# Optimization experiments

Measured on AMD Instinct MI355X. Metric: run time of the kernel, lower is better.

Reference implementation:

```python
import jax, jax.numpy as jnp
import numpy as np

N_EMBD = 512
HEAD_SIZE = 64
END_TOKEN = 32000  # == vocab_size


def setup_inputs() -> dict:
    key = jax.random.key(0)
    k1, k2, k3, k4, k5 = jax.random.split(key, 5)
    B, T = 16, 2048
    x = jax.random.normal(k1, (B, T, N_EMBD), dtype=jnp.float32)
    idx = jax.random.randint(k2, (B, T), 0, END_TOKEN)  # never hits END_TOKEN
    s = 1.0 / np.sqrt(N_EMBD)
    Wk = jax.random.normal(k3, (N_EMBD, HEAD_SIZE), dtype=jnp.float32) * s
    Wq = jax.random.normal(k4, (N_EMBD, HEAD_SIZE), dtype=jnp.float32) * s
    Wv = jax.random.normal(k5, (N_EMBD, HEAD_SIZE), dtype=jnp.float32) * s
    return {"x": x, "Wk": Wk, "Wq": Wq, "Wv": Wv, "idx": idx}


def reference(x, Wk, Wq, Wv, idx):
    B, T, C = x.shape
    k = x @ Wk  # [B,T,H]
    q = x @ Wq
    v = x @ Wv
    # end-token mask: zero out query rows at positions >= first end-token position
    is_end = idx == END_TOKEN                       # [B,T]
    has_end = jnp.any(is_end, axis=1)               # [B]
    first_end = jnp.argmax(is_end, axis=1)          # [B], 0 if none
    pos = jnp.arange(T)
    row_ok = jnp.where(has_end[:, None], pos[None, :] < first_end[:, None], True)  # [B,T]
    causal = jnp.tril(jnp.ones((T, T), dtype=bool))
    mask = causal[None, :, :] & row_ok[:, :, None]  # [B,T,T]
    # NOTE: original scales by C**-0.5 with C = n_embd, not head_size
    wei = jnp.einsum('bqh,bkh->bqk', q, k) * (C ** -0.5)
    wei = jnp.where(mask, wei, -jnp.inf)
    wei = jax.nn.softmax(wei, axis=-1)
    out = jnp.einsum('bqk,bkh->bqh', wei, v)  # [B,T,H]
    return out
```

## Files before the change

### kernel.cpp

```cpp
#include <hip/hip_runtime.h>
#include <hip/hip_bf16.h>


#define B_ 16
#define T_ 2048
#define C_ 512

typedef __attribute__((ext_vector_type(4))) float f32x4;
typedef __attribute__((ext_vector_type(8))) short bf16x8;
typedef __attribute__((ext_vector_type(4))) unsigned int u32x4;

__device__ inline unsigned short f2bf(float f) {
    unsigned int u = __builtin_bit_cast(unsigned int, f);
    u += 0x7fff + ((u >> 16) & 1);
    return (unsigned short)(u >> 16);
}

__device__ inline unsigned int cvt_pk_bf16(float lo, float hi) {
    unsigned int r;
    asm("v_cvt_pk_bf16_f32 %0, %1, %2" : "=v"(r) : "v"(lo), "v"(hi));
    return r;
}

__device__ inline f32x4 mfma16(bf16x8 a, bf16x8 b, f32x4 c) {
    return __builtin_amdgcn_mfma_f32_16x16x32_bf16(a, b, c, 0, 0, 0);
}

__global__ void prep_kernel(const float* __restrict__ Wk, const float* __restrict__ Wq,
                            const float* __restrict__ Wv, unsigned short* __restrict__ Wt,
                            const int* __restrict__ idx, int* __restrict__ pbmin) {
    if (blockIdx.x >= 384) {
        __shared__ int wmin[4];
        int bid = blockIdx.x - 384;
        int i = bid * 256 + threadIdx.x;
        int val = (idx[i] == 32000) ? (i & 2047) : T_;
#pragma unroll
        for (int off = 1; off < 64; off <<= 1)
            val = min(val, __shfl_xor(val, off));
        int wave = threadIdx.x >> 6, lane = threadIdx.x & 63;
        if (lane == 0) wmin[wave] = val;
        __syncthreads();
        if (threadIdx.x == 0)
            pbmin[bid] = min(min(wmin[0], wmin[1]), min(wmin[2], wmin[3]));
        return;
    }
    int id = blockIdx.x * 256 + threadIdx.x;
    int n = id >> 9, k = id & 511;
    int mtx = n >> 6, nl = n & 63;
    const float* W = (mtx == 0) ? Wk : ((mtx == 1) ? Wq : Wv);
    float v = W[k * 64 + nl];
    if (mtx == 1) v *= 0.0637587166f;
    Wt[n * 512 + k] = f2bf(v);
}

__global__ __launch_bounds__(256) void qkv_kernel(
        const float* __restrict__ x, const unsigned short* __restrict__ Wt,
        unsigned short* __restrict__ Qm, unsigned short* __restrict__ Km,
        unsigned short* __restrict__ Vt) {
    __shared__ __align__(16) char smem[32768];
    unsigned short* xs  = (unsigned short*)smem;
    unsigned short* wsh = (unsigned short*)(smem + 8192);
    unsigned short* co  = (unsigned short*)smem;
    unsigned short* vco = (unsigned short*)(smem + 17408);

    int tid = threadIdx.x, wave = tid >> 6, lane = tid & 63;
    int m16 = lane & 15, quad = lane >> 4;
    int row0 = blockIdx.x * 64;

    int xrow[2], xcol[2], wrow[6], wcol[6];
#pragma unroll
    for (int i = 0; i < 2; i++) { int u = tid + i * 256; xrow[i] = u >> 3; xcol[i] = (u & 7) * 8; }
#pragma unroll
    for (int i = 0; i < 6; i++) { int u = tid + i * 256; wrow[i] = u >> 3; wcol[i] = (u & 7) * 8; }

    f32x4 xa[2][2]; bf16x8 wr[6];
#pragma unroll
    for (int i = 0; i < 2; i++) {
        const f32x4* p = (const f32x4*)(x + (long)(row0 + xrow[i]) * C_ + xcol[i]);
        xa[i][0] = p[0]; xa[i][1] = p[1];
    }
#pragma unroll
    for (int i = 0; i < 6; i++) wr[i] = *(const bf16x8*)&Wt[wrow[i] * C_ + wcol[i]];

    f32x4 ka[4], qa[4], va[4];
#pragma unroll
    for (int i = 0; i < 4; i++) {
        ka[i] = (f32x4){0.f, 0.f, 0.f, 0.f};
        qa[i] = (f32x4){0.f, 0.f, 0.f, 0.f};
        va[i] = (f32x4){0.f, 0.f, 0.f, 0.f};
    }

    for (int kb = 0; kb < C_; kb += 64) {
        __syncthreads();
#pragma unroll
        for (int i = 0; i < 2; i++) {
            u32x4 t;
            t[0] = cvt_pk_bf16(xa[i][0][0], xa[i][0][1]);
            t[1] = cvt_pk_bf16(xa[i][0][2], xa[i][0][3]);
            t[2] = cvt_pk_bf16(xa[i][1][0], xa[i][1][1]);
            t[3] = cvt_pk_bf16(xa[i][1][2], xa[i][1][3]);
            *(u32x4*)&xs[xrow[i] * 64 + (xcol[i] ^ ((xrow[i] & 7) * 8))] = t;
        }
#pragma unroll
        for (int i = 0; i < 6; i++)
            *(bf16x8*)&wsh[wrow[i] * 64 + (wcol[i] ^ ((wrow[i] & 7) * 8))] = wr[i];
        __syncthreads();
        int kn = kb + 64;
        if (kn < C_) {
#pragma unroll
            for (int i = 0; i < 2; i++) {
                const f32x4* p = (const f32x4*)(x + (long)(row0 + xrow[i]) * C_ + kn + xcol[i]);
                xa[i][0] = p[0]; xa[i][1] = p[1];
            }
#pragma unroll
            for (int i = 0; i < 6; i++) wr[i] = *(const bf16x8*)&Wt[wrow[i] * C_ + kn + wcol[i]];
        }
#pragma unroll
        for (int ks = 0; ks < 2; ks++) {
            int ko = ks * 32 + quad * 8;
            bf16x8 xf[4];
#pragma unroll
            for (int mt = 0; mt < 4; mt++) {
                int ar = mt * 16 + m16;
                xf[mt] = *(const bf16x8*)&xs[ar * 64 + (ko ^ ((ar & 7) * 8))];
            }
            int kr = wave * 16 + m16, qr = 64 + wave * 16 + m16, vr = 128 + wave * 16 + m16;
            bf16x8 wk = *(const bf16x8*)&wsh[kr * 64 + (ko ^ ((kr & 7) * 8))];
            bf16x8 wq = *(const bf16x8*)&wsh[qr * 64 + (ko ^ ((qr & 7) * 8))];
            bf16x8 wv = *(const bf16x8*)&wsh[vr * 64 + (ko ^ ((vr & 7) * 8))];
#pragma unroll
            for (int mt = 0; mt < 4; mt++) ka[mt] = mfma16(xf[mt], wk, ka[mt]);
#pragma unroll
            for (int mt = 0; mt < 4; mt++) qa[mt] = mfma16(xf[mt], wq, qa[mt]);
#pragma unroll
            for (int mt = 0; mt < 4; mt++) va[mt] = mfma16(wv, xf[mt], va[mt]);
        }
    }
    __syncthreads();

#pragma unroll
    for (int mt = 0; mt < 4; mt++) {
        int trow = mt * 16 + quad * 4;
#pragma unroll
        for (int r = 0; r < 4; r++) {
            co[(trow + r) * 136 + wave * 16 + m16]      = f2bf(ka[mt][r]);
            co[(trow + r) * 136 + 64 + wave * 16 + m16] = f2bf(qa[mt][r]);
            vco[wave * 1152 + (quad * 4 + r) * 72 + mt * 16 + m16] = f2bf(va[mt][r]);
        }
    }
    __syncthreads();
#pragma unroll
    for (int i = 0; i < 4; i++) {
        int u = tid + i * 256; int tok = u >> 4; int fg = u & 15;
        bf16x8 vv = *(const bf16x8*)&co[tok * 136 + fg * 8];
        unsigned short* dst = (fg < 8) ? Km : Qm;
        *(bf16x8*)&dst[(long)(row0 + tok) * 64 + (fg & 7) * 8] = vv;
    }
    int bb = row0 >> 11, tl = row0 & 2047;
#pragma unroll
    for (int i = 0; i < 2; i++) {
        int u = lane + i * 64; int hl = u >> 3; int tg = u & 7;
        bf16x8 vv = *(const bf16x8*)&vco[wave * 1152 + hl * 72 + tg * 8];
        *(bf16x8*)&Vt[((long)bb * 64 + wave * 16 + hl) * T_ + tl + tg * 8] = vv;
    }
}

__global__ __launch_bounds__(512, 4) void attn_kernel(
        const unsigned short* __restrict__ Qm, const unsigned short* __restrict__ Km,
        const unsigned short* __restrict__ Vt, const int* __restrict__ pbmin,
        float* __restrict__ out) {
    __shared__ __align__(16) unsigned short Klds[2][2][64 * 64];
    __shared__ __align__(16) unsigned short Vlds[2][2][64 * 64];
    __shared__ __align__(16) unsigned short Plds[8][16 * 64];

    int id = blockIdx.x;
    int j = id & 255, hi = id >> 8;
    int qt = hi ? 31 - (j >> 3) : (j >> 3);
    int b = (j & 7) | (hi << 3);

    int tid = threadIdx.x, wave = tid >> 6, lane = tid & 63;
    int g = wave >> 2, wg = wave & 3;
    int m16 = lane & 15, quad = lane >> 4;
    int row0 = qt * 64;
    long bT = (long)b * T_;

    int n = qt + 1;
    int n0 = (n + 1) >> 1;
    int n1 = n - n0;
    int ng = g ? n1 : n0;
    int kbase = g ? n0 : 0;
    int nloop = n0;

    int gtid = wg * 64 + lane;
    int srow[2], sk8[2], ssw[2];
#pragma unroll
    for (int c = 0; c < 2; c++) {
        int cc = gtid + c * 256;
        srow[c] = cc >> 3; sk8[c] = (cc & 7) * 8;
        ssw[c] = sk8[c] ^ ((srow[c] & 7) * 8);
    }

    const unsigned short* qp = Qm + (bT + row0 + wg * 16 + m16) * 64;
    bf16x8 qf0 = *(const bf16x8*)(qp + quad * 8);
    bf16x8 qf1 = *(const bf16x8*)(qp + 32 + quad * 8);

    f32x4 o[5];
#pragma unroll
    for (int h = 0; h < 5; h++) o[h] = (f32x4){0.f, 0.f, 0.f, 0.f};
    int qloc = row0 + wg * 16 + quad * 4;

    bf16x8 onesb;
    {
        short ov = (m16 == 0) ? (short)0x3F80 : (short)0;
#pragma unroll
        for (int jj = 0; jj < 8; jj++) onesb[jj] = ov;
    }

    unsigned short (*Kg)[64 * 64] = Klds[g];
    unsigned short (*Vg)[64 * 64] = Vlds[g];

    bf16x8 kp[2], vp[2];
    if (ng > 0) {
        long c0 = (long)kbase * 64;
#pragma unroll
        for (int c = 0; c < 2; c++) {
            kp[c] = *(const bf16x8*)&Km[(bT + c0 + srow[c]) * 64 + sk8[c]];
            vp[c] = *(const bf16x8*)&Vt[((long)b * 64 + srow[c]) * T_ + c0 + sk8[c]];
        }
#pragma unroll
        for (int c = 0; c < 2; c++) {
            *(bf16x8*)&Kg[0][srow[c] * 64 + ssw[c]] = kp[c];
            *(bf16x8*)&Vg[0][srow[c] * 64 + ssw[c]] = vp[c];
        }
    }

    for (int it = 0; it < nloop; ++it) {
        int cur = it & 1;
        bool active = it < ng;
        int kt = kbase + it;
        bool pf = active && (it + 1 < ng);
        __syncthreads();
        if (pf) {
            long cn = (long)(kt + 1) * 64;
#pragma unroll
            for (int c = 0; c < 2; c++) {
                kp[c] = *(const bf16x8*)&Km[(bT + cn + srow[c]) * 64 + sk8[c]];
                vp[c] = *(const bf16x8*)&Vt[((long)b * 64 + srow[c]) * T_ + cn + sk8[c]];
            }
        }
        if (active) {
            const unsigned short* Kb = Kg[cur];
            const unsigned short* Vb = Vg[cur];

            f32x4 s[4];
#pragma unroll
            for (int ns = 0; ns < 4; ns++) {
                int krow = ns * 16 + m16;
                int swz = (krow & 7) * 8;
                bf16x8 kf0 = *(const bf16x8*)&Kb[krow * 64 + ((quad * 8) ^ swz)];
                bf16x8 kf1 = *(const bf16x8*)&Kb[krow * 64 + ((32 + quad * 8) ^ swz)];
                f32x4 z = (f32x4){0.f, 0.f, 0.f, 0.f};
                z = mfma16(qf0, kf0, z);
                z = mfma16(qf1, kf1, z);
                s[ns] = z;
            }

            bool diag = (kt == qt);
            if (diag) {
#pragma unroll
                for (int r = 0; r < 4; r++) {
                    int qpos = qloc + r;
#pragma unroll
                    for (int ns = 0; ns < 4; ns++) {
                        int nn = kt * 64 + ns * 16 + m16;
                        if (nn > qpos) s[ns][r] = -20.0f;
                    }
                }
            }
#pragma unroll
            for (int ns = 0; ns < 4; ns++)
#pragma unroll
                for (int r = 0; r < 4; r++)
                    s[ns][r] = exp2f(s[ns][r]);

            unsigned short* pw = Plds[wave];
#pragma unroll
            for (int r = 0; r < 4; r++) {
                int mrow = quad * 4 + r;
                int swzr = (mrow & 7) * 8;
                unsigned int p01 = cvt_pk_bf16(s[0][r], s[1][r]);
                unsigned int p23 = cvt_pk_bf16(s[2][r], s[3][r]);
                pw[mrow * 64 + ((m16) ^ swzr)]      = (unsigned short)(p01 & 0xffffu);
                pw[mrow * 64 + ((16 + m16) ^ swzr)] = (unsigned short)(p01 >> 16);
                pw[mrow * 64 + ((32 + m16) ^ swzr)] = (unsigned short)(p23 & 0xffffu);
                pw[mrow * 64 + ((48 + m16) ^ swzr)] = (unsigned short)(p23 >> 16);
            }

            int aswz = (m16 & 7) * 8;
            bf16x8 pa0 = *(const bf16x8*)&pw[m16 * 64 + ((quad * 8) ^ aswz)];
            bf16x8 pa1 = *(const bf16x8*)&pw[m16 * 64 + ((32 + quad * 8) ^ aswz)];
#pragma unroll
            for (int hs = 0; hs < 4; hs++) {
                int vrow = hs * 16 + m16;
                int vswz = (vrow & 7) * 8;
                bf16x8 vb0 = *(const bf16x8*)&Vb[vrow * 64 + ((quad * 8) ^ vswz)];
                bf16x8 vb1 = *(const bf16x8*)&Vb[vrow * 64 + ((32 + quad * 8) ^ vswz)];
                o[hs] = mfma16(pa0, vb0, o[hs]);
                o[hs] = mfma16(pa1, vb1, o[hs]);
            }
            o[4] = mfma16(pa0, onesb, o[4]);
            o[4] = mfma16(pa1, onesb, o[4]);
        }
        if (pf) {
            int nxt = 1 - cur;
#pragma unroll
            for (int c = 0; c < 2; c++) {
                *(bf16x8*)&Kg[nxt][srow[c] * 64 + ssw[c]] = kp[c];
                *(bf16x8*)&Vg[nxt][srow[c] * 64 + ssw[c]] = vp[c];
            }
        }
    }

    __syncthreads();
    float* Po = (float*)&Klds[0][0][0];
    float* Pl = Po + 64 * 68;
    if (g == 1) {
#pragma unroll
        for (int r = 0; r < 4; r++) {
            int row = wg * 16 + quad * 4 + r;
#pragma unroll
            for (int hs = 0; hs < 4; hs++)
                Po[row * 68 + hs * 16 + m16] = o[hs][r];
            if (m16 == 0) Pl[row] = o[4][r];
        }
    }
    __syncthreads();
    if (g == 0) {
        int feb = T_;
#pragma unroll
        for (int c = 0; c < 8; c++) feb = min(feb, pbmin[b * 8 + c]);
#pragma unroll
        for (int r = 0; r < 4; r++) {
            int row = wg * 16 + quad * 4 + r;
            int t = row0 + row;
            float l0 = __shfl(o[4][r], lane & 48);
            float inv = 1.0f / (l0 + Pl[row]);
            bool dead = (t >= feb);
#pragma unroll
            for (int hs = 0; hs < 4; hs++) {
                float val = dead ? __builtin_nanf("")
                                 : (o[hs][r] + Po[row * 68 + hs * 16 + m16]) * inv;
                out[(bT + t) * 64 + hs * 16 + m16] = val;
            }
        }
    }
}

extern "C" void kernel_launch(void* const* d_in, const int* in_sizes, int n_in,
                              void* d_out, int out_size, void* d_ws, size_t ws_size,
                              hipStream_t stream) {
    const float* x  = (const float*)d_in[0];
    const float* Wk = (const float*)d_in[1];
    const float* Wq = (const float*)d_in[2];
    const float* Wv = (const float*)d_in[3];
    const int* idx  = (const int*)d_in[4];
    float* out = (float*)d_out;

    char* ws = (char*)d_ws;
    int* pbmin         = (int*)ws;
    unsigned short* Wt = (unsigned short*)(ws + 1024);
    unsigned short* Qm = (unsigned short*)(ws + 262144);
    unsigned short* Km = (unsigned short*)(ws + 262144 + 4194304);
    unsigned short* Vt = (unsigned short*)(ws + 262144 + 8388608);

    prep_kernel<<<512, 256, 0, stream>>>(Wk, Wq, Wv, Wt, idx, pbmin);
    qkv_kernel<<<512, 256, 0, stream>>>(x, Wt, Qm, Km, Vt);
    attn_kernel<<<512, 512, 0, stream>>>(Qm, Km, Vt, pbmin, out);
}
```

Measured before the change: 133.9 us.

## Split QKV projection K-dimension across two wave groups with LDS reduction

The QKV projection kernel now runs 512 threads per block, with two groups of four waves, each handling half of the 512-wide reduction dimension. Each group has its own LDS staging area. Partial accumulators from group 1 are written to LDS and summed by group 0 before the bf16 store. This halves the serial K-loop length per wave and raises the number of waves in flight, at the cost of more LDS (75 KB), an extra reduction pass, and loss of the register prefetch of weights.

```diff
diff --git a/kernel.cpp b/kernel.cpp
--- a/kernel.cpp
+++ b/kernel.cpp
@@ -53,34 +53,34 @@
     Wt[n * 512 + k] = f2bf(v);
 }
 
-__global__ __launch_bounds__(256) void qkv_kernel(
+__global__ __launch_bounds__(512, 4) void qkv_kernel(
         const float* __restrict__ x, const unsigned short* __restrict__ Wt,
         unsigned short* __restrict__ Qm, unsigned short* __restrict__ Km,
         unsigned short* __restrict__ Vt) {
-    __shared__ __align__(16) char smem[32768];
-    unsigned short* xs  = (unsigned short*)smem;
-    unsigned short* wsh = (unsigned short*)(smem + 8192);
-    unsigned short* co  = (unsigned short*)smem;
-    unsigned short* vco = (unsigned short*)(smem + 17408);
+    __shared__ __align__(16) char smem[76800];
+    unsigned short* xs  = (unsigned short*)(smem + (threadIdx.x >> 8 >= 1 ? 32768 : 0));
+    unsigned short* wsh = (unsigned short*)(smem + (threadIdx.x >> 8 >= 1 ? 32768 : 0) + 8192);
+    float* msc          = (float*)smem;
+    unsigned short* co  = (unsigned short*)(smem + 49152);
+    unsigned short* vco = (unsigned short*)(smem + 49152 + 17408);
 
     int tid = threadIdx.x, wave = tid >> 6, lane = tid & 63;
+    int g = wave >> 2, wg = wave & 3;
+    int gtid = wg * 64 + lane;
     int m16 = lane & 15, quad = lane >> 4;
     int row0 = blockIdx.x * 64;
-
-    int xrow[2], xcol[2], wrow[6], wcol[6];
-#pragma unroll
-    for (int i = 0; i < 2; i++) { int u = tid + i * 256; xrow[i] = u >> 3; xcol[i] = (u & 7) * 8; }
-#pragma unroll
-    for (int i = 0; i < 6; i++) { int u = tid + i * 256; wrow[i] = u >> 3; wcol[i] = (u & 7) * 8; }
-
-    f32x4 xa[2][2]; bf16x8 wr[6];
+    int kbase = g * 256;
+
+    int xrow[2], xcol[2];
+#pragma unroll
+    for (int i = 0; i < 2; i++) { int u = gtid + i * 256; xrow[i] = u >> 3; xcol[i] = (u & 7) * 8; }
+
+    f32x4 xa[2][2];
 #pragma unroll
     for (int i = 0; i < 2; i++) {
-        const f32x4* p = (const f32x4*)(x + (long)(row0 + xrow[i]) * C_ + xcol[i]);
+        const f32x4* p = (const f32x4*)(x + (long)(row0 + xrow[i]) * C_ + kbase + xcol[i]);
         xa[i][0] = p[0]; xa[i][1] = p[1];
     }
-#pragma unroll
-    for (int i = 0; i < 6; i++) wr[i] = *(const bf16x8*)&Wt[wrow[i] * C_ + wcol[i]];
 
     f32x4 ka[4], qa[4], va[4];
 #pragma unroll
@@ -90,8 +90,30 @@
         va[i] = (f32x4){0.f, 0.f, 0.f, 0.f};
     }
 
-    for (int kb = 0; kb < C_; kb += 64) {
+    for (int c = 0; c < 4; c++) {
+        int kb = kbase + c * 64;
+        bf16x8 wrA[3];
+#pragma unroll
+        for (int i = 0; i < 3; i++) {
+            int u = gtid + i * 256;
+            wrA[i] = *(const bf16x8*)&Wt[(u >> 3) * C_ + kb + (u & 7) * 8];
+        }
         __syncthreads();
+#pragma unroll
+        for (int i = 0; i < 3; i++) {
+            int u = gtid + i * 256; int wr_ = u >> 3, wc = (u & 7) * 8;
+            *(bf16x8*)&wsh[wr_ * 64 + (wc ^ ((wr_ & 7) * 8))] = wrA[i];
+        }
+#pragma unroll
+        for (int i = 0; i < 3; i++) {
+            int u = gtid + (3 + i) * 256;
+            wrA[i] = *(const bf16x8*)&Wt[(u >> 3) * C_ + kb + (u & 7) * 8];
+        }
+#pragma unroll
+        for (int i = 0; i < 3; i++) {
+            int u = gtid + (3 + i) * 256; int wr_ = u >> 3, wc = (u & 7) * 8;
+            *(bf16x8*)&wsh[wr_ * 64 + (wc ^ ((wr_ & 7) * 8))] = wrA[i];
+        }
 #pragma unroll
         for (int i = 0; i < 2; i++) {
             u32x4 t;
@@ -101,19 +123,13 @@
             t[3] = cvt_pk_bf16(xa[i][1][2], xa[i][1][3]);
             *(u32x4*)&xs[xrow[i] * 64 + (xcol[i] ^ ((xrow[i] & 7) * 8))] = t;
         }
-#pragma unroll
-        for (int i = 0; i < 6; i++)
-            *(bf16x8*)&wsh[wrow[i] * 64 + (wcol[i] ^ ((wrow[i] & 7) * 8))] = wr[i];
         __syncthreads();
-        int kn = kb + 64;
-        if (kn < C_) {
+        if (c < 3) {
 #pragma unroll
             for (int i = 0; i < 2; i++) {
-                const f32x4* p = (const f32x4*)(x + (long)(row0 + xrow[i]) * C_ + kn + xcol[i]);
+                const f32x4* p = (const f32x4*)(x + (long)(row0 + xrow[i]) * C_ + kb + 64 + xcol[i]);
                 xa[i][0] = p[0]; xa[i][1] = p[1];
             }
-#pragma unroll
-            for (int i = 0; i < 6; i++) wr[i] = *(const bf16x8*)&Wt[wrow[i] * C_ + kn + wcol[i]];
         }
 #pragma unroll
         for (int ks = 0; ks < 2; ks++) {
@@ -124,7 +140,7 @@
                 int ar = mt * 16 + m16;
                 xf[mt] = *(const bf16x8*)&xs[ar * 64 + (ko ^ ((ar & 7) * 8))];
             }
-            int kr = wave * 16 + m16, qr = 64 + wave * 16 + m16, vr = 128 + wave * 16 + m16;
+            int kr = wg * 16 + m16, qr = 64 + wg * 16 + m16, vr = 128 + wg * 16 + m16;
             bf16x8 wk = *(const bf16x8*)&wsh[kr * 64 + (ko ^ ((kr & 7) * 8))];
             bf16x8 wq = *(const bf16x8*)&wsh[qr * 64 + (ko ^ ((qr & 7) * 8))];
             bf16x8 wv = *(const bf16x8*)&wsh[vr * 64 + (ko ^ ((vr & 7) * 8))];
@@ -136,32 +152,46 @@
             for (int mt = 0; mt < 4; mt++) va[mt] = mfma16(wv, xf[mt], va[mt]);
         }
     }
+
     __syncthreads();
-
-#pragma unroll
-    for (int mt = 0; mt < 4; mt++) {
-        int trow = mt * 16 + quad * 4;
-#pragma unroll
-        for (int r = 0; r < 4; r++) {
-            co[(trow + r) * 136 + wave * 16 + m16]      = f2bf(ka[mt][r]);
-            co[(trow + r) * 136 + 64 + wave * 16 + m16] = f2bf(qa[mt][r]);
-            vco[wave * 1152 + (quad * 4 + r) * 72 + mt * 16 + m16] = f2bf(va[mt][r]);
+    if (g == 1) {
+        f32x4* dst = (f32x4*)msc + gtid * 12;
+#pragma unroll
+        for (int mt = 0; mt < 4; mt++) {
+            dst[mt] = ka[mt]; dst[4 + mt] = qa[mt]; dst[8 + mt] = va[mt];
         }
     }
     __syncthreads();
-#pragma unroll
-    for (int i = 0; i < 4; i++) {
-        int u = tid + i * 256; int tok = u >> 4; int fg = u & 15;
+    if (g == 0) {
+        const f32x4* src = (const f32x4*)msc + gtid * 12;
+#pragma unroll
+        for (int mt = 0; mt < 4; mt++) {
+            ka[mt] += src[mt]; qa[mt] += src[4 + mt]; va[mt] += src[8 + mt];
+        }
+#pragma unroll
+        for (int mt = 0; mt < 4; mt++) {
+            int trow = mt * 16 + quad * 4;
+#pragma unroll
+            for (int r = 0; r < 4; r++) {
+                co[(trow + r) * 136 + wg * 16 + m16]      = f2bf(ka[mt][r]);
+                co[(trow + r) * 136 + 64 + wg * 16 + m16] = f2bf(qa[mt][r]);
+                vco[wg * 1152 + (quad * 4 + r) * 72 + mt * 16 + m16] = f2bf(va[mt][r]);
+            }
+        }
+    }
+    __syncthreads();
+#pragma unroll
+    for (int i = 0; i < 2; i++) {
+        int u = tid + i * 512; int tok = u >> 4; int fg = u & 15;
         bf16x8 vv = *(const bf16x8*)&co[tok * 136 + fg * 8];
         unsigned short* dst = (fg < 8) ? Km : Qm;
         *(bf16x8*)&dst[(long)(row0 + tok) * 64 + (fg & 7) * 8] = vv;
     }
     int bb = row0 >> 11, tl = row0 & 2047;
-#pragma unroll
-    for (int i = 0; i < 2; i++) {
-        int u = lane + i * 64; int hl = u >> 3; int tg = u & 7;
-        bf16x8 vv = *(const bf16x8*)&vco[wave * 1152 + hl * 72 + tg * 8];
-        *(bf16x8*)&Vt[((long)bb * 64 + wave * 16 + hl) * T_ + tl + tg * 8] = vv;
+    {
+        int hl = tid >> 3, tg = tid & 7;
+        bf16x8 vv = *(const bf16x8*)&vco[(hl >> 4) * 1152 + (hl & 15) * 72 + tg * 8];
+        *(bf16x8*)&Vt[((long)bb * 64 + hl) * T_ + tl + tg * 8] = vv;
     }
 }
 
@@ -374,6 +404,6 @@
     unsigned short* Vt = (unsigned short*)(ws + 262144 + 8388608);
 
     prep_kernel<<<512, 256, 0, stream>>>(Wk, Wq, Wv, Wt, idx, pbmin);
-    qkv_kernel<<<512, 256, 0, stream>>>(x, Wt, Qm, Km, Vt);
+    qkv_kernel<<<512, 512, 0, stream>>>(x, Wt, Qm, Km, Vt);
     attn_kernel<<<512, 512, 0, stream>>>(Qm, Km, Vt, pbmin, out);
 }
```

Result: slower. 138.5 us (+3.5%).

## Double-buffer LDS tiles in QKV projection to drop one barrier per k-step

Applied to the files above, without the earlier changes.

The QKV projection kernel now keeps two LDS buffers for the x and W tiles. The next chunk is written into the alternate buffer after the MFMAs on the current one, so each k-iteration needs one __syncthreads instead of two. Swizzled LDS offsets are precomputed once outside the loop. Shared memory per block doubles to 64KB, which may reduce the number of blocks resident per CU.

```diff
diff --git a/kernel.cpp b/kernel.cpp
--- a/kernel.cpp
+++ b/kernel.cpp
@@ -57,9 +57,7 @@
         const float* __restrict__ x, const unsigned short* __restrict__ Wt,
         unsigned short* __restrict__ Qm, unsigned short* __restrict__ Km,
         unsigned short* __restrict__ Vt) {
-    __shared__ __align__(16) char smem[32768];
-    unsigned short* xs  = (unsigned short*)smem;
-    unsigned short* wsh = (unsigned short*)(smem + 8192);
+    __shared__ __align__(16) char smem[65536];
     unsigned short* co  = (unsigned short*)smem;
     unsigned short* vco = (unsigned short*)(smem + 17408);
 
@@ -67,16 +65,25 @@
     int m16 = lane & 15, quad = lane >> 4;
     int row0 = blockIdx.x * 64;
 
-    int xrow[2], xcol[2], wrow[6], wcol[6];
-#pragma unroll
-    for (int i = 0; i < 2; i++) { int u = tid + i * 256; xrow[i] = u >> 3; xcol[i] = (u & 7) * 8; }
-#pragma unroll
-    for (int i = 0; i < 6; i++) { int u = tid + i * 256; wrow[i] = u >> 3; wcol[i] = (u & 7) * 8; }
+    int xrow[2], xoff[2], wrow[6], wcol[6], woff[6];
+#pragma unroll
+    for (int i = 0; i < 2; i++) {
+        int u = tid + i * 256; xrow[i] = u >> 3; int xc = (u & 7) * 8;
+        xoff[i] = xrow[i] * 64 + (xc ^ ((xrow[i] & 7) * 8));
+    }
+#pragma unroll
+    for (int i = 0; i < 6; i++) {
+        int u = tid + i * 256; wrow[i] = u >> 3; wcol[i] = (u & 7) * 8;
+        woff[i] = wrow[i] * 64 + (wcol[i] ^ ((wrow[i] & 7) * 8));
+    }
+    int xgcol[2];
+#pragma unroll
+    for (int i = 0; i < 2; i++) xgcol[i] = ((tid + i * 256) & 7) * 8;
 
     f32x4 xa[2][2]; bf16x8 wr[6];
 #pragma unroll
     for (int i = 0; i < 2; i++) {
-        const f32x4* p = (const f32x4*)(x + (long)(row0 + xrow[i]) * C_ + xcol[i]);
+        const f32x4* p = (const f32x4*)(x + (long)(row0 + xrow[i]) * C_ + xgcol[i]);
         xa[i][0] = p[0]; xa[i][1] = p[1];
     }
 #pragma unroll
@@ -90,8 +97,9 @@
         va[i] = (f32x4){0.f, 0.f, 0.f, 0.f};
     }
 
-    for (int kb = 0; kb < C_; kb += 64) {
-        __syncthreads();
+    {
+        unsigned short* xs0  = (unsigned short*)smem;
+        unsigned short* wsh0 = (unsigned short*)(smem + 16384);
 #pragma unroll
         for (int i = 0; i < 2; i++) {
             u32x4 t;
@@ -99,17 +107,23 @@
             t[1] = cvt_pk_bf16(xa[i][0][2], xa[i][0][3]);
             t[2] = cvt_pk_bf16(xa[i][1][0], xa[i][1][1]);
             t[3] = cvt_pk_bf16(xa[i][1][2], xa[i][1][3]);
-            *(u32x4*)&xs[xrow[i] * 64 + (xcol[i] ^ ((xrow[i] & 7) * 8))] = t;
-        }
-#pragma unroll
-        for (int i = 0; i < 6; i++)
-            *(bf16x8*)&wsh[wrow[i] * 64 + (wcol[i] ^ ((wrow[i] & 7) * 8))] = wr[i];
+            *(u32x4*)&xs0[xoff[i]] = t;
+        }
+#pragma unroll
+        for (int i = 0; i < 6; i++) *(bf16x8*)&wsh0[woff[i]] = wr[i];
+    }
+
+    for (int c = 0; c < 8; c++) {
+        int cur = c & 1;
+        unsigned short* xs  = (unsigned short*)(smem + cur * 8192);
+        unsigned short* wsh = (unsigned short*)(smem + 16384 + cur * 24576);
         __syncthreads();
-        int kn = kb + 64;
-        if (kn < C_) {
+        int kn = (c + 1) * 64;
+        bool pf = (kn < C_);
+        if (pf) {
 #pragma unroll
             for (int i = 0; i < 2; i++) {
-                const f32x4* p = (const f32x4*)(x + (long)(row0 + xrow[i]) * C_ + kn + xcol[i]);
+                const f32x4* p = (const f32x4*)(x + (long)(row0 + xrow[i]) * C_ + kn + xgcol[i]);
                 xa[i][0] = p[0]; xa[i][1] = p[1];
             }
 #pragma unroll
@@ -134,6 +148,21 @@
             for (int mt = 0; mt < 4; mt++) qa[mt] = mfma16(xf[mt], wq, qa[mt]);
 #pragma unroll
             for (int mt = 0; mt < 4; mt++) va[mt] = mfma16(wv, xf[mt], va[mt]);
+        }
+        if (pf) {
+            unsigned short* xsn  = (unsigned short*)(smem + (1 - cur) * 8192);
+            unsigned short* wshn = (unsigned short*)(smem + 16384 + (1 - cur) * 24576);
+#pragma unroll
+            for (int i = 0; i < 2; i++) {
+                u32x4 t;
+                t[0] = cvt_pk_bf16(xa[i][0][0], xa[i][0][1]);
+                t[1] = cvt_pk_bf16(xa[i][0][2], xa[i][0][3]);
+                t[2] = cvt_pk_bf16(xa[i][1][0], xa[i][1][1]);
+                t[3] = cvt_pk_bf16(xa[i][1][2], xa[i][1][3]);
+                *(u32x4*)&xsn[xoff[i]] = t;
+            }
+#pragma unroll
+            for (int i = 0; i < 6; i++) *(bf16x8*)&wshn[woff[i]] = wr[i];
         }
     }
     __syncthreads();
```

Result: no change. 135.8 us (+1.4%).
